# Optimization experiments

Hardware: AMD Instinct MI355X
Metric: run time of the kernel (lower is better)

The kernel has to match this reference:

```python
import jax, jax.numpy as jnp
import numpy as np

B, N, K = 4, 50000, 128   # batch, surface points, deformation nodes
GD = 128                  # SDF grid resolution (D=H=W)


def setup_inputs() -> dict:
    key = jax.random.key(0)
    ks = jax.random.split(key, 7)
    constants = jax.random.normal(ks[0], (B, K), dtype=jnp.float32)
    scales = 0.05 + 0.25 * jax.random.uniform(ks[1], (B, K), dtype=jnp.float32)
    # proper-ish rotations via QR of random matrices
    M = jax.random.normal(ks[2], (B, K, 3, 3), dtype=jnp.float32)
    rotations, _ = jnp.linalg.qr(M)
    centers = jax.random.uniform(ks[3], (B, K, 3), dtype=jnp.float32, minval=-0.5, maxval=0.5)
    surface_samples = jax.random.uniform(ks[4], (B, N, 6), dtype=jnp.float32, minval=-0.5, maxval=0.5)
    grid = jax.random.normal(ks[5], (B, GD, GD, GD), dtype=jnp.float32)
    # world2grid maps world [-0.5,0.5] -> grid index [0, GD-1]
    w2g = np.zeros((B, 4, 4), dtype=np.float32)
    w2g[:, 0, 0] = w2g[:, 1, 1] = w2g[:, 2, 2] = float(GD - 1)
    w2g[:, :3, 3] = float(GD - 1) / 2.0
    w2g[:, 3, 3] = 1.0
    world2grid = jnp.asarray(w2g)
    return {"constants": constants, "scales": scales, "rotations": rotations,
            "centers": centers, "surface_samples": surface_samples,
            "grid": grid, "world2grid": world2grid}


def _trilinear_border(vol, xyz):
    """torch grid_sample (5D, bilinear, align_corners=True, border) for one batch.
    vol: (D,H,W); xyz: (N,3) normalized coords in [-1,1], order (x,y,z)."""
    D, H, W = vol.shape
    x = jnp.clip((xyz[:, 0] + 1.0) * 0.5 * (W - 1), 0.0, W - 1)
    y = jnp.clip((xyz[:, 1] + 1.0) * 0.5 * (H - 1), 0.0, H - 1)
    z = jnp.clip((xyz[:, 2] + 1.0) * 0.5 * (D - 1), 0.0, D - 1)
    x0 = jnp.floor(x); y0 = jnp.floor(y); z0 = jnp.floor(z)
    fx = x - x0; fy = y - y0; fz = z - z0
    x0i = x0.astype(jnp.int32); x1i = jnp.minimum(x0i + 1, W - 1)
    y0i = y0.astype(jnp.int32); y1i = jnp.minimum(y0i + 1, H - 1)
    z0i = z0.astype(jnp.int32); z1i = jnp.minimum(z0i + 1, D - 1)
    c000 = vol[z0i, y0i, x0i]; c001 = vol[z0i, y0i, x1i]
    c010 = vol[z0i, y1i, x0i]; c011 = vol[z0i, y1i, x1i]
    c100 = vol[z1i, y0i, x0i]; c101 = vol[z1i, y0i, x1i]
    c110 = vol[z1i, y1i, x0i]; c111 = vol[z1i, y1i, x1i]
    c00 = c000 * (1 - fx) + c001 * fx
    c01 = c010 * (1 - fx) + c011 * fx
    c10 = c100 * (1 - fx) + c101 * fx
    c11 = c110 * (1 - fx) + c111 * fx
    c0 = c00 * (1 - fy) + c01 * fy
    c1 = c10 * (1 - fy) + c11 * fy
    return c0 * (1 - fz) + c1 * fz


def reference(constants, scales, rotations, centers, surface_samples, grid, world2grid):
    pts = surface_samples[..., :3]                       # (B,N,3)
    diff = pts[:, :, None, :] - centers[:, None, :, :]   # (B,N,K,3)  == p - t_source
    d2 = jnp.sum(diff * diff, axis=-1)                   # (B,N,K)
    # sample_rbf_weights with use_constants=True
    w = jnp.exp(-d2 / (2.0 * scales * scales)[:, None, :]) * (constants * constants)[:, None, :]
    w = w / jnp.sum(w, axis=-1, keepdims=True)           # normalize over nodes

    # target = roll batch by -1 (source_idx+1 mod B)
    R_t = jnp.roll(rotations, -1, axis=0)
    R_rel = jnp.einsum('bkij,bklj->bkil', R_t, rotations)       # R_target @ R_source^T
    c_t = jnp.roll(centers, -1, axis=0)
    transformed = jnp.einsum('bkij,bnkj->bnki', R_rel, diff) + c_t[:, None, :, :]
    blended = jnp.einsum('bnk,bnki->bni', w, transformed)        # (B,N,3)

    w2g_t = jnp.roll(world2grid, -1, axis=0)
    A = w2g_t[:, :3, :3]
    t = w2g_t[:, :3, 3]
    gcs = jnp.einsum('bij,bnj->bni', A, blended) + t[:, None, :]  # grid coords (x,y,z)

    D, H, W = grid.shape[1], grid.shape[2], grid.shape[3]
    denom = jnp.array([W - 1, H - 1, D - 1], dtype=gcs.dtype)
    gcs = 2.0 * (gcs / denom) - 1.0                               # normalize to [-1,1]

    grid_t = jnp.roll(grid, -1, axis=0)
    sdf = jax.vmap(_trilinear_border)(grid_t, gcs)                # (B,N)
    return jnp.sum(jnp.mean(sdf * sdf, axis=1))
```

## Files before the change

kernel.cpp:

```cpp
#include <hip/hip_runtime.h>

#define K_   128
#define GD_  128
#define PPT  4

static __device__ __forceinline__ float fast_exp2(float x) {
#if __has_builtin(__builtin_amdgcn_exp2f)
    return __builtin_amdgcn_exp2f(x);
#else
    return exp2f(x);
#endif
}

__global__ __launch_bounds__(64) void surf_loss_kernel(
    const float* __restrict__ constants,
    const float* __restrict__ scales,
    const float* __restrict__ rotations,
    const float* __restrict__ centers,
    const float* __restrict__ sp,
    const float* __restrict__ grid,
    const float* __restrict__ w2g,
    float* __restrict__ out,
    int N, int B, int bpb)
{
    __shared__ float lds[K_ * 20];
    const int tid = threadIdx.x;
    const int blk = blockIdx.x;
    const int b   = blk / bpb;
    const int i0  = (blk - b * bpb) * (64 * PPT);
    const int bn  = (b + 1 == B) ? 0 : (b + 1);
    const float L2E = 1.4426950408889634f;

    for (int k = tid; k < K_; k += 64) {
        const float* R  = rotations + (size_t)(b  * K_ + k) * 9;
        const float* Rt = rotations + (size_t)(bn * K_ + k) * 9;
        float m[9];
#pragma unroll
        for (int i = 0; i < 3; ++i)
#pragma unroll
            for (int l = 0; l < 3; ++l)
                m[i * 3 + l] = Rt[i * 3 + 0] * R[l * 3 + 0]
                             + Rt[i * 3 + 1] * R[l * 3 + 1]
                             + Rt[i * 3 + 2] * R[l * 3 + 2];
        const float* c  = centers + (size_t)(b  * K_ + k) * 3;
        const float* ct = centers + (size_t)(bn * K_ + k) * 3;
        float c0 = c[0], c1 = c[1], c2v = c[2];
        float sig = scales[b * K_ + k];
        float s   = 1.0f / (2.0f * sig * sig);
        float con = constants[b * K_ + k];
        float csq = con * con;
        float s2n = -s * L2E;
        float r   = log2f(csq) + s2n * (c0 * c0 + c1 * c1 + c2v * c2v);

        float* o = lds + k * 20;
        o[0] = m[0]; o[1] = m[1]; o[2] = m[2];
        o[3] = m[3]; o[4] = m[4]; o[5] = m[5];
        o[6] = m[6]; o[7] = m[7]; o[8] = m[8];
        o[9]  = ct[0] - (m[0] * c0 + m[1] * c1 + m[2] * c2v);
        o[10] = ct[1] - (m[3] * c0 + m[4] * c1 + m[5] * c2v);
        o[11] = ct[2] - (m[6] * c0 + m[7] * c1 + m[8] * c2v);
        o[12] = -2.0f * s2n * c0;
        o[13] = -2.0f * s2n * c1;
        o[14] = -2.0f * s2n * c2v;
        o[15] = r;
        o[16] = s2n;
        o[17] = 0.f; o[18] = 0.f; o[19] = 0.f;
    }
    __syncthreads();

    const float* Aw = w2g + (size_t)bn * 16;
    const float A00 = Aw[0], A01 = Aw[1],  A02 = Aw[2],  T0 = Aw[3];
    const float A10 = Aw[4], A11 = Aw[5],  A12 = Aw[6],  T1 = Aw[7];
    const float A20 = Aw[8], A21 = Aw[9],  A22 = Aw[10], T2 = Aw[11];

    float px[PPT], py[PPT], pz[PPT], pq[PPT];
    float ax[PPT], ay[PPT], az[PPT], aw[PPT];
    bool  valid[PPT];
    const float* spb = sp + (size_t)b * N * 6;
#pragma unroll
    for (int j = 0; j < PPT; ++j) {
        int n = i0 + tid + 64 * j;
        valid[j] = (n < N);
        int nn = valid[j] ? n : 0;
        const float* q = spb + (size_t)nn * 6;
        px[j] = q[0]; py[j] = q[1]; pz[j] = q[2];
        pq[j] = px[j] * px[j] + py[j] * py[j] + pz[j] * pz[j];
        ax[j] = 0.f; ay[j] = 0.f; az[j] = 0.f; aw[j] = 0.f;
    }

#pragma unroll 2
    for (int k = 0; k < K_; ++k) {
        const float4* f = (const float4*)(lds + k * 20);
        const float4 f0 = f[0];
        const float4 f1 = f[1];
        const float4 f2 = f[2];
        const float4 f3 = f[3];
        const float  s2 = lds[k * 20 + 16];
#pragma unroll
        for (int j = 0; j < PPT; ++j) {
            float e = f3.w + f3.x * px[j] + f3.y * py[j] + f3.z * pz[j] + s2 * pq[j];
            float w = fast_exp2(e);
            float tx = f2.y + f0.x * px[j] + f0.y * py[j] + f0.z * pz[j];
            float ty = f2.z + f0.w * px[j] + f1.x * py[j] + f1.y * pz[j];
            float tz = f2.w + f1.z * px[j] + f1.w * py[j] + f2.x * pz[j];
            ax[j] += w * tx;
            ay[j] += w * ty;
            az[j] += w * tz;
            aw[j] += w;
        }
    }

    const float* gb = grid + (size_t)bn * GD_ * GD_ * GD_;
    float accum = 0.0f;
#pragma unroll
    for (int j = 0; j < PPT; ++j) {
        if (!valid[j]) continue;
        float inv = 1.0f / aw[j];
        float bx = ax[j] * inv, by = ay[j] * inv, bz = az[j] * inv;
        float gx = A00 * bx + A01 * by + A02 * bz + T0;
        float gy = A10 * bx + A11 * by + A12 * bz + T1;
        float gz = A20 * bx + A21 * by + A22 * bz + T2;
        const float invD = 1.0f / (float)(GD_ - 1);
        gx = 2.0f * (gx * invD) - 1.0f;
        gy = 2.0f * (gy * invD) - 1.0f;
        gz = 2.0f * (gz * invD) - 1.0f;
        float x = fminf(fmaxf((gx + 1.0f) * 0.5f * (GD_ - 1), 0.0f), (float)(GD_ - 1));
        float y = fminf(fmaxf((gy + 1.0f) * 0.5f * (GD_ - 1), 0.0f), (float)(GD_ - 1));
        float z = fminf(fmaxf((gz + 1.0f) * 0.5f * (GD_ - 1), 0.0f), (float)(GD_ - 1));
        float x0f = floorf(x), y0f = floorf(y), z0f = floorf(z);
        float fx = x - x0f, fy = y - y0f, fz = z - z0f;
        int x0 = (int)x0f, y0 = (int)y0f, z0 = (int)z0f;
        int x1 = x0 + 1 > GD_ - 1 ? GD_ - 1 : x0 + 1;
        int y1 = y0 + 1 > GD_ - 1 ? GD_ - 1 : y0 + 1;
        int z1 = z0 + 1 > GD_ - 1 ? GD_ - 1 : z0 + 1;
        int zy00 = (z0 * GD_ + y0) * GD_;
        int zy01 = (z0 * GD_ + y1) * GD_;
        int zy10 = (z1 * GD_ + y0) * GD_;
        int zy11 = (z1 * GD_ + y1) * GD_;
        float c000 = gb[zy00 + x0], c001 = gb[zy00 + x1];
        float c010 = gb[zy01 + x0], c011 = gb[zy01 + x1];
        float c100 = gb[zy10 + x0], c101 = gb[zy10 + x1];
        float c110 = gb[zy11 + x0], c111 = gb[zy11 + x1];
        float ofx = 1.0f - fx, ofy = 1.0f - fy, ofz = 1.0f - fz;
        float c00 = c000 * ofx + c001 * fx;
        float c01 = c010 * ofx + c011 * fx;
        float c10 = c100 * ofx + c101 * fx;
        float c11 = c110 * ofx + c111 * fx;
        float c0 = c00 * ofy + c01 * fy;
        float c1 = c10 * ofy + c11 * fy;
        float sdf = c0 * ofz + c1 * fz;
        accum += sdf * sdf;
    }

#pragma unroll
    for (int off = 32; off > 0; off >>= 1)
        accum += __shfl_down(accum, off, 64);
    if (tid == 0)
        atomicAdd(out, accum * (1.0f / (float)N));
}

extern "C" void kernel_launch(void* const* d_in, const int* in_sizes, int n_in,
                              void* d_out, int out_size, void* d_ws, size_t ws_size,
                              hipStream_t stream) {
    const float* constants = (const float*)d_in[0];
    const float* scales    = (const float*)d_in[1];
    const float* rotations = (const float*)d_in[2];
    const float* centers   = (const float*)d_in[3];
    const float* sp        = (const float*)d_in[4];
    const float* grid      = (const float*)d_in[5];
    const float* w2g       = (const float*)d_in[6];
    float* out = (float*)d_out;

    const int B = in_sizes[6] / 16;
    const int N = in_sizes[4] / (6 * B);

    hipMemsetAsync(out, 0, sizeof(float), stream);

    const int ppb = 64 * PPT;
    const int bpb = (N + ppb - 1) / ppb;
    dim3 g(B * bpb), blkdim(64);
    hipLaunchKernelGGL(surf_loss_kernel, g, blkdim, 0, stream,
                       constants, scales, rotations, centers, sp, grid, w2g, out,
                       N, B, bpb);
}
```

Before: 131.5 us.

## Precompute per-node params in separate kernel and fold grid affine into them

Moves the per-node rotation and center precomputation into a separate kernel that writes to workspace. It folds the world2grid affine and the normalize/denormalize round trip into the per-node matrices, so the main kernel works directly in grid coordinates. The main kernel now uses 256-thread blocks with one point per thread, reads params from global memory (scalar, uniform loads) instead of LDS, and reduces per block through shared memory. Tradeoffs: an extra kernel launch, losing the 4-points-per-thread reuse of each loaded param, and a slightly different floating-point rounding order.

```diff
diff --git a/kernel.cpp b/kernel.cpp
--- a/kernel.cpp
+++ b/kernel.cpp
@@ -2,7 +2,7 @@
 
 #define K_   128
 #define GD_  128
-#define PPT  4
+#define PSTR 20
 
 static __device__ __forceinline__ float fast_exp2(float x) {
 #if __has_builtin(__builtin_amdgcn_exp2f)
@@ -12,127 +12,125 @@
 #endif
 }
 
-__global__ __launch_bounds__(64) void surf_loss_kernel(
+__global__ void surf_param_kernel(
     const float* __restrict__ constants,
     const float* __restrict__ scales,
     const float* __restrict__ rotations,
     const float* __restrict__ centers,
+    const float* __restrict__ w2g,
+    float* __restrict__ params,
+    int B)
+{
+    int idx = blockIdx.x * blockDim.x + threadIdx.x;
+    if (idx >= B * K_) return;
+    int b = idx / K_, k = idx - b * K_;
+    int bn = (b + 1 == B) ? 0 : (b + 1);
+    const float L2E = 1.4426950408889634f;
+
+    const float* R  = rotations + (size_t)(b  * K_ + k) * 9;
+    const float* Rt = rotations + (size_t)(bn * K_ + k) * 9;
+    float m[9];
+#pragma unroll
+    for (int i = 0; i < 3; ++i)
+#pragma unroll
+        for (int l = 0; l < 3; ++l)
+            m[i * 3 + l] = Rt[i * 3 + 0] * R[l * 3 + 0]
+                         + Rt[i * 3 + 1] * R[l * 3 + 1]
+                         + Rt[i * 3 + 2] * R[l * 3 + 2];
+
+    const float* Aw = w2g + (size_t)bn * 16;
+    float G[9], A[9] = {Aw[0], Aw[1], Aw[2], Aw[4], Aw[5], Aw[6], Aw[8], Aw[9], Aw[10]};
+    float T[3] = {Aw[3], Aw[7], Aw[11]};
+#pragma unroll
+    for (int i = 0; i < 3; ++i)
+#pragma unroll
+        for (int l = 0; l < 3; ++l)
+            G[i * 3 + l] = A[i * 3 + 0] * m[0 * 3 + l]
+                         + A[i * 3 + 1] * m[1 * 3 + l]
+                         + A[i * 3 + 2] * m[2 * 3 + l];
+
+    const float* c  = centers + (size_t)(b  * K_ + k) * 3;
+    const float* ct = centers + (size_t)(bn * K_ + k) * 3;
+    float c0 = c[0], c1 = c[1], c2 = c[2];
+    float vw0 = ct[0] - (m[0] * c0 + m[1] * c1 + m[2] * c2);
+    float vw1 = ct[1] - (m[3] * c0 + m[4] * c1 + m[5] * c2);
+    float vw2 = ct[2] - (m[6] * c0 + m[7] * c1 + m[8] * c2);
+    float v0 = A[0] * vw0 + A[1] * vw1 + A[2] * vw2 + T[0];
+    float v1 = A[3] * vw0 + A[4] * vw1 + A[5] * vw2 + T[1];
+    float v2 = A[6] * vw0 + A[7] * vw1 + A[8] * vw2 + T[2];
+
+    float sig = scales[b * K_ + k];
+    float s   = 1.0f / (2.0f * sig * sig);
+    float con = constants[b * K_ + k];
+    float s2n = -s * L2E;
+    float r   = log2f(con * con) + s2n * (c0 * c0 + c1 * c1 + c2 * c2);
+
+    float* o = params + (size_t)idx * PSTR;
+    o[0] = G[0]; o[1] = G[1]; o[2] = G[2]; o[3] = G[3];
+    o[4] = G[4]; o[5] = G[5]; o[6] = G[6]; o[7] = G[7];
+    o[8] = G[8]; o[9] = v0;  o[10] = v1;  o[11] = v2;
+    o[12] = -2.0f * s2n * c0;
+    o[13] = -2.0f * s2n * c1;
+    o[14] = -2.0f * s2n * c2;
+    o[15] = r;
+    o[16] = s2n;
+    o[17] = 0.f; o[18] = 0.f; o[19] = 0.f;
+}
+
+__global__ __launch_bounds__(256) void surf_loss_kernel(
     const float* __restrict__ sp,
     const float* __restrict__ grid,
-    const float* __restrict__ w2g,
+    const float* __restrict__ params,
     float* __restrict__ out,
     int N, int B, int bpb)
 {
-    __shared__ float lds[K_ * 20];
     const int tid = threadIdx.x;
     const int blk = blockIdx.x;
     const int b   = blk / bpb;
-    const int i0  = (blk - b * bpb) * (64 * PPT);
+    const int n   = (blk - b * bpb) * 256 + tid;
+    const bool valid = (n < N);
     const int bn  = (b + 1 == B) ? 0 : (b + 1);
-    const float L2E = 1.4426950408889634f;
 
-    for (int k = tid; k < K_; k += 64) {
-        const float* R  = rotations + (size_t)(b  * K_ + k) * 9;
-        const float* Rt = rotations + (size_t)(bn * K_ + k) * 9;
-        float m[9];
-#pragma unroll
-        for (int i = 0; i < 3; ++i)
-#pragma unroll
-            for (int l = 0; l < 3; ++l)
-                m[i * 3 + l] = Rt[i * 3 + 0] * R[l * 3 + 0]
-                             + Rt[i * 3 + 1] * R[l * 3 + 1]
-                             + Rt[i * 3 + 2] * R[l * 3 + 2];
-        const float* c  = centers + (size_t)(b  * K_ + k) * 3;
-        const float* ct = centers + (size_t)(bn * K_ + k) * 3;
-        float c0 = c[0], c1 = c[1], c2v = c[2];
-        float sig = scales[b * K_ + k];
-        float s   = 1.0f / (2.0f * sig * sig);
-        float con = constants[b * K_ + k];
-        float csq = con * con;
-        float s2n = -s * L2E;
-        float r   = log2f(csq) + s2n * (c0 * c0 + c1 * c1 + c2v * c2v);
+    const float* qp = sp + ((size_t)b * N + (valid ? n : 0)) * 6;
+    float px = qp[0], py = qp[1], pz = qp[2];
+    float pq = px * px + py * py + pz * pz;
+    float ax = 0.f, ay = 0.f, az = 0.f, aw = 0.f;
 
-        float* o = lds + k * 20;
-        o[0] = m[0]; o[1] = m[1]; o[2] = m[2];
-        o[3] = m[3]; o[4] = m[4]; o[5] = m[5];
-        o[6] = m[6]; o[7] = m[7]; o[8] = m[8];
-        o[9]  = ct[0] - (m[0] * c0 + m[1] * c1 + m[2] * c2v);
-        o[10] = ct[1] - (m[3] * c0 + m[4] * c1 + m[5] * c2v);
-        o[11] = ct[2] - (m[6] * c0 + m[7] * c1 + m[8] * c2v);
-        o[12] = -2.0f * s2n * c0;
-        o[13] = -2.0f * s2n * c1;
-        o[14] = -2.0f * s2n * c2v;
-        o[15] = r;
-        o[16] = s2n;
-        o[17] = 0.f; o[18] = 0.f; o[19] = 0.f;
-    }
-    __syncthreads();
+    const float* P = params + (size_t)b * K_ * PSTR;
+#pragma unroll 2
+    for (int k = 0; k < K_; ++k) {
+        const float* o = P + k * PSTR;
+        float g00 = o[0], g01 = o[1], g02 = o[2];
+        float g10 = o[3], g11 = o[4], g12 = o[5];
+        float g20 = o[6], g21 = o[7], g22 = o[8];
+        float v0  = o[9], v1 = o[10], v2 = o[11];
+        float q0  = o[12], q1 = o[13], q2 = o[14];
+        float r   = o[15], s2n = o[16];
 
-    const float* Aw = w2g + (size_t)bn * 16;
-    const float A00 = Aw[0], A01 = Aw[1],  A02 = Aw[2],  T0 = Aw[3];
-    const float A10 = Aw[4], A11 = Aw[5],  A12 = Aw[6],  T1 = Aw[7];
-    const float A20 = Aw[8], A21 = Aw[9],  A22 = Aw[10], T2 = Aw[11];
-
-    float px[PPT], py[PPT], pz[PPT], pq[PPT];
-    float ax[PPT], ay[PPT], az[PPT], aw[PPT];
-    bool  valid[PPT];
-    const float* spb = sp + (size_t)b * N * 6;
-#pragma unroll
-    for (int j = 0; j < PPT; ++j) {
-        int n = i0 + tid + 64 * j;
-        valid[j] = (n < N);
-        int nn = valid[j] ? n : 0;
-        const float* q = spb + (size_t)nn * 6;
-        px[j] = q[0]; py[j] = q[1]; pz[j] = q[2];
-        pq[j] = px[j] * px[j] + py[j] * py[j] + pz[j] * pz[j];
-        ax[j] = 0.f; ay[j] = 0.f; az[j] = 0.f; aw[j] = 0.f;
+        float e = r + q0 * px + q1 * py + q2 * pz + s2n * pq;
+        float w = fast_exp2(e);
+        float tx = v0 + g00 * px + g01 * py + g02 * pz;
+        float ty = v1 + g10 * px + g11 * py + g12 * pz;
+        float tz = v2 + g20 * px + g21 * py + g22 * pz;
+        ax += w * tx;
+        ay += w * ty;
+        az += w * tz;
+        aw += w;
     }
 
-#pragma unroll 2
-    for (int k = 0; k < K_; ++k) {
-        const float4* f = (const float4*)(lds + k * 20);
-        const float4 f0 = f[0];
-        const float4 f1 = f[1];
-        const float4 f2 = f[2];
-        const float4 f3 = f[3];
-        const float  s2 = lds[k * 20 + 16];
-#pragma unroll
-        for (int j = 0; j < PPT; ++j) {
-            float e = f3.w + f3.x * px[j] + f3.y * py[j] + f3.z * pz[j] + s2 * pq[j];
-            float w = fast_exp2(e);
-            float tx = f2.y + f0.x * px[j] + f0.y * py[j] + f0.z * pz[j];
-            float ty = f2.z + f0.w * px[j] + f1.x * py[j] + f1.y * pz[j];
-            float tz = f2.w + f1.z * px[j] + f1.w * py[j] + f2.x * pz[j];
-            ax[j] += w * tx;
-            ay[j] += w * ty;
-            az[j] += w * tz;
-            aw[j] += w;
-        }
-    }
-
-    const float* gb = grid + (size_t)bn * GD_ * GD_ * GD_;
     float accum = 0.0f;
-#pragma unroll
-    for (int j = 0; j < PPT; ++j) {
-        if (!valid[j]) continue;
-        float inv = 1.0f / aw[j];
-        float bx = ax[j] * inv, by = ay[j] * inv, bz = az[j] * inv;
-        float gx = A00 * bx + A01 * by + A02 * bz + T0;
-        float gy = A10 * bx + A11 * by + A12 * bz + T1;
-        float gz = A20 * bx + A21 * by + A22 * bz + T2;
-        const float invD = 1.0f / (float)(GD_ - 1);
-        gx = 2.0f * (gx * invD) - 1.0f;
-        gy = 2.0f * (gy * invD) - 1.0f;
-        gz = 2.0f * (gz * invD) - 1.0f;
-        float x = fminf(fmaxf((gx + 1.0f) * 0.5f * (GD_ - 1), 0.0f), (float)(GD_ - 1));
-        float y = fminf(fmaxf((gy + 1.0f) * 0.5f * (GD_ - 1), 0.0f), (float)(GD_ - 1));
-        float z = fminf(fmaxf((gz + 1.0f) * 0.5f * (GD_ - 1), 0.0f), (float)(GD_ - 1));
+    if (valid) {
+        float inv = 1.0f / aw;
+        float x = fminf(fmaxf(ax * inv, 0.0f), (float)(GD_ - 1));
+        float y = fminf(fmaxf(ay * inv, 0.0f), (float)(GD_ - 1));
+        float z = fminf(fmaxf(az * inv, 0.0f), (float)(GD_ - 1));
         float x0f = floorf(x), y0f = floorf(y), z0f = floorf(z);
         float fx = x - x0f, fy = y - y0f, fz = z - z0f;
         int x0 = (int)x0f, y0 = (int)y0f, z0 = (int)z0f;
         int x1 = x0 + 1 > GD_ - 1 ? GD_ - 1 : x0 + 1;
         int y1 = y0 + 1 > GD_ - 1 ? GD_ - 1 : y0 + 1;
         int z1 = z0 + 1 > GD_ - 1 ? GD_ - 1 : z0 + 1;
+        const float* gb = grid + (size_t)bn * GD_ * GD_ * GD_;
         int zy00 = (z0 * GD_ + y0) * GD_;
         int zy01 = (z0 * GD_ + y1) * GD_;
         int zy10 = (z1 * GD_ + y0) * GD_;
@@ -149,14 +147,18 @@
         float c0 = c00 * ofy + c01 * fy;
         float c1 = c10 * ofy + c11 * fy;
         float sdf = c0 * ofz + c1 * fz;
-        accum += sdf * sdf;
+        accum = sdf * sdf;
     }
 
+    __shared__ float red[4];
 #pragma unroll
     for (int off = 32; off > 0; off >>= 1)
         accum += __shfl_down(accum, off, 64);
+    int wave = tid >> 6;
+    if ((tid & 63) == 0) red[wave] = accum;
+    __syncthreads();
     if (tid == 0)
-        atomicAdd(out, accum * (1.0f / (float)N));
+        atomicAdd(out, (red[0] + red[1] + red[2] + red[3]) * (1.0f / (float)N));
 }
 
 extern "C" void kernel_launch(void* const* d_in, const int* in_sizes, int n_in,
@@ -170,16 +172,18 @@
     const float* grid      = (const float*)d_in[5];
     const float* w2g       = (const float*)d_in[6];
     float* out = (float*)d_out;
+    float* params = (float*)d_ws;
 
     const int B = in_sizes[6] / 16;
     const int N = in_sizes[4] / (6 * B);
 
     hipMemsetAsync(out, 0, sizeof(float), stream);
 
-    const int ppb = 64 * PPT;
-    const int bpb = (N + ppb - 1) / ppb;
-    dim3 g(B * bpb), blkdim(64);
-    hipLaunchKernelGGL(surf_loss_kernel, g, blkdim, 0, stream,
-                       constants, scales, rotations, centers, sp, grid, w2g, out,
-                       N, B, bpb);
+    int np = B * K_;
+    hipLaunchKernelGGL(surf_param_kernel, dim3((np + 255) / 256), dim3(256), 0, stream,
+                       constants, scales, rotations, centers, w2g, params, B);
+
+    const int bpb = (N + 255) / 256;
+    hipLaunchKernelGGL(surf_loss_kernel, dim3(B * bpb), dim3(256), 0, stream,
+                       sp, grid, params, out, N, B, bpb);
 }
```

New measurement: 123.1 us. 1.07x faster.
